# Kernel optimization log

Measured on AMD Instinct MI355X. Metric: run time of the kernel, lower is better.

## Reference

```python
import jax, jax.numpy as jnp
import numpy as np

G = 13            # grid_size
A = 5             # num_anchors
C = 36            # num_classes
OBJ_SCALE = 5.0
NOOBJ_SCALE = 1.0
CLASS_SCALE = 1.0
COORD_SCALE = 1.0
ANCHORS = jnp.array([[1.08, 1.19], [3.42, 4.41], [6.63, 11.38], [9.42, 5.11], [16.62, 10.52]], dtype=jnp.float32)


def setup_inputs() -> dict:
    key = jax.random.key(0)
    k1, k2, k3 = jax.random.split(key, 3)
    B, T = 1024, 30
    predictions = jax.random.normal(k1, (B, A * (5 + C), G, G), dtype=jnp.float32)
    # x,y,w,h normalized to (0,1); class id in [0,C) stored as float in channel 4
    xywh = jax.random.uniform(k2, (B, T, 4), dtype=jnp.float32, minval=1e-3, maxval=0.999)
    cls = jax.random.randint(k3, (B, T, 1), 0, C).astype(jnp.float32)
    target = jnp.concatenate([xywh, cls], axis=-1)
    return {"predictions": predictions, "target": target}


def build_targets(target):
    # target: [B, T, 5]  (x, y, w, h, class), x/y/w/h in [0,1)
    B, T, _ = target.shape
    valid = jnp.sum(target, axis=-1) != 0                      # [B, T]
    gx = target[..., 0] * G
    gy = target[..., 1] * G
    gw = target[..., 2] * G
    gh = target[..., 3] * G
    gi = gx.astype(jnp.int32)                                  # int() truncation (values >= 0)
    gj = gy.astype(jnp.int32)
    # anchor IoU for boxes centered at origin: inter = min(w)*min(h)
    aw = ANCHORS[:, 0]                                          # [A]
    ah = ANCHORS[:, 1]
    inter = jnp.minimum(gw[..., None], aw) * jnp.minimum(gh[..., None], ah)   # [B,T,A]
    union = (gw * gh)[..., None] + aw * ah - inter
    iou = inter / (union + 1e-16)
    best_n = jnp.argmax(iou, axis=-1)                           # [B, T] first-max, matches torch loop
    baw = ANCHORS[best_n, 0]
    bah = ANCHORS[best_n, 1]
    tx = gx - gi.astype(gx.dtype)
    ty = gy - gj.astype(gy.dtype)
    tw = jnp.log(gw / baw + 1e-16)
    th = jnp.log(gh / bah + 1e-16)
    cls_idx = target[..., 4].astype(jnp.int32)                  # [B, T]

    N = B * A * G * G
    b_idx = jnp.arange(B, dtype=jnp.int32)[:, None]             # [B,1] -> broadcast to [B,T]
    flat = ((b_idx * A + best_n.astype(jnp.int32)) * G + gj) * G + gi   # [B,T]
    flat = jnp.where(valid, flat, N)                            # out-of-bounds -> dropped
    flat = flat.reshape(-1)                                     # [B*T]

    conf_mask = jnp.full((N,), NOOBJ_SCALE, dtype=jnp.float32).at[flat].set(OBJ_SCALE, mode="drop")
    coord_mask = jnp.zeros((N, 4), dtype=jnp.float32).at[flat].set(1.0, mode="drop")
    class_mask = jnp.zeros((N, C), dtype=jnp.float32).at[flat].set(CLASS_SCALE, mode="drop")
    tconf = jnp.zeros((N,), dtype=jnp.float32).at[flat].set(1.0, mode="drop")
    tcoord_vals = jnp.stack([tx, ty, tw, th], axis=-1).reshape(-1, 4)
    tcoord = jnp.zeros((N, 4), dtype=jnp.float32).at[flat].set(tcoord_vals, mode="drop")
    tclass = jnp.zeros((N, C), dtype=jnp.float32).at[flat, cls_idx.reshape(-1)].set(1.0, mode="drop")

    shp = (B, A, G, G)
    return (coord_mask.reshape(shp + (4,)), conf_mask.reshape(shp), class_mask.reshape(shp + (C,)),
            tcoord.reshape(shp + (4,)), tconf.reshape(shp), tclass.reshape(shp + (C,)))


def reference(predictions, target):
    B = predictions.shape[0]
    p = predictions.reshape(B, A, 5 + C, G, G).transpose(0, 1, 3, 4, 2)   # [B,A,G,G,5+C]
    coord_mask, conf_mask, class_mask, tcoord, tconf, tclass = build_targets(target)
    pred_coord = p[..., 1:5]
    pred_conf = jax.nn.sigmoid(p[..., 0])
    pred_class = p[..., 5:]
    loss_coord = COORD_SCALE * jnp.sum((pred_coord * coord_mask - tcoord * coord_mask) ** 2) / B
    loss_conf = jnp.sum((pred_conf * conf_mask - tconf * conf_mask) ** 2) / B
    labels = jnp.argmax(tclass.reshape(-1, C), axis=1)
    logp = jax.nn.log_softmax(pred_class.reshape(-1, C), axis=-1)
    loss_class = CLASS_SCALE * (-jnp.take_along_axis(logp, labels[:, None], axis=1).sum()) / B
    total_loss = loss_coord + loss_conf + loss_class
    return (total_loss, loss_coord, loss_conf, loss_class)
```

## Files before the change

### kernel.cpp

```cpp
#include <hip/hip_runtime.h>

#define GQ 13
#define AQ 5
#define CQ 36
#define TQ 30
#define CH (5 + CQ)
#define GG (GQ * GQ)
#define PLANE (CH * GG)
#define BLOCK 256
#define NVEC 6
#define VEC_DWORDS (NVEC * BLOCK * 4)


__global__ __launch_bounds__(BLOCK) void yolo_plane(
    const float* __restrict__ pred,
    const float* __restrict__ target,
    float* __restrict__ ws, int nb)
{
    __shared__ float s_plane[PLANE];
    __shared__ int   s_info[GG];
    __shared__ int   s_cell[TQ];
    __shared__ float s_tc[TQ][4];
    __shared__ int   s_cls[TQ];
    __shared__ float s_red[3][BLOCK / 64];

    const int a   = blockIdx.x;
    const int b   = blockIdx.y;
    const int bid = b * AQ + a;
    const int tid = threadIdx.x;

    const float* src = pred + ((size_t)b * AQ + a) * PLANE;
    float4 vv[NVEC];
    #pragma unroll
    for (int r = 0; r < NVEC; r++)
        __builtin_memcpy(&vv[r], src + (size_t)(tid + BLOCK * r) * 4, 16);
    float tl[4]; int ntl = 0;
    #pragma unroll
    for (int r = 0; r < 4; r++) {
        int i = VEC_DWORDS + tid + BLOCK * r;
        if (i < PLANE) { tl[r] = src[i]; ntl = r + 1; }
    }

    if (tid < TQ) {
        const float* tg = target + ((size_t)b * TQ + tid) * 5;
        float x = tg[0], y = tg[1], w = tg[2], h = tg[3], c5 = tg[4];
        bool valid = (x + y + w + h + c5) != 0.0f;
        float gx = x * GQ, gy = y * GQ, gw = w * GQ, gh = h * GQ;
        int gi = (int)gx, gj = (int)gy;
        const float AW[5] = {1.08f, 3.42f, 6.63f, 9.42f, 16.62f};
        const float AH[5] = {1.19f, 4.41f, 11.38f, 5.11f, 10.52f};
        float best = -1.0f; int bn = 0;
        #pragma unroll
        for (int k = 0; k < AQ; k++) {
            float inter = fminf(gw, AW[k]) * fminf(gh, AH[k]);
            float un    = gw * gh + AW[k] * AH[k] - inter;
            float iou   = inter / (un + 1e-16f);
            if (iou > best) { best = iou; bn = k; }
        }
        s_cell[tid]  = valid ? ((bn * GQ + gj) * GQ + gi) : -1;
        s_tc[tid][0] = gx - (float)gi;
        s_tc[tid][1] = gy - (float)gj;
        s_tc[tid][2] = __logf(gw / AW[bn] + 1e-16f);
        s_tc[tid][3] = __logf(gh / AH[bn] + 1e-16f);
        s_cls[tid]   = (int)c5;
    }
    if (tid < GG) s_info[tid] = 0;

    #pragma unroll
    for (int r = 0; r < NVEC; r++)
        __builtin_memcpy(&s_plane[(tid + BLOCK * r) * 4], &vv[r], 16);
    #pragma unroll
    for (int r = 0; r < 4; r++)
        if (r < ntl) s_plane[VEC_DWORDS + tid + BLOCK * r] = tl[r];
    __syncthreads();

    if (tid == 0) {
        #pragma unroll 1
        for (int t = 0; t < TQ; t++) {
            int c = s_cell[t] - a * GG;
            if (c >= 0 && c < GG) {
                int lab = s_cls[t];
                int old = s_info[c];
                if (old) lab = min(lab, old & 0xff);
                s_info[c] = 0x40000000 | (t << 8) | lab;
            }
        }
    }
    __syncthreads();

    float lcoord = 0.0f, lconf = 0.0f, lclass = 0.0f;
    if (tid < GG) {
        int info = s_info[tid];

        float p0  = s_plane[tid];
        float sig = 1.0f / (1.0f + __expf(-p0));
        float d   = info ? 5.0f * (sig - 1.0f) : sig;
        lconf = d * d;

        if (info) {
            int t = (info >> 8) & 0xff;
            float d1 = s_plane[1 * GG + tid] - s_tc[t][0];
            float d2 = s_plane[2 * GG + tid] - s_tc[t][1];
            float d3 = s_plane[3 * GG + tid] - s_tc[t][2];
            float d4 = s_plane[4 * GG + tid] - s_tc[t][3];
            lcoord = d1 * d1 + d2 * d2 + d3 * d3 + d4 * d4;
        }

        int lab = info & 0xff;
        const float* cb = s_plane + 5 * GG + tid;
        float sum = 0.0f, vl = 0.0f;
        #pragma unroll
        for (int c = 0; c < CQ; c++) {
            float v = cb[(size_t)c * GG];
            sum += __expf(v);
            vl = (c == lab) ? v : vl;
        }
        lclass = __logf(sum) - vl;
    }

    #pragma unroll
    for (int off = 32; off > 0; off >>= 1) {
        lcoord += __shfl_down(lcoord, off, 64);
        lconf  += __shfl_down(lconf,  off, 64);
        lclass += __shfl_down(lclass, off, 64);
    }
    int wv = tid >> 6, ln = tid & 63;
    if (ln == 0) { s_red[0][wv] = lcoord; s_red[1][wv] = lconf; s_red[2][wv] = lclass; }
    __syncthreads();
    if (tid == 0) {
        float a0 = 0.f, a1 = 0.f, a2 = 0.f;
        #pragma unroll
        for (int w = 0; w < BLOCK / 64; w++) {
            a0 += s_red[0][w]; a1 += s_red[1][w]; a2 += s_red[2][w];
        }
        ws[0 * nb + bid] = a0;
        ws[1 * nb + bid] = a1;
        ws[2 * nb + bid] = a2;
    }
}

__global__ __launch_bounds__(BLOCK) void yolo_reduce(
    const float* __restrict__ ws, float* __restrict__ out, int nb, float invB)
{
    __shared__ float s_red[3][BLOCK / 64];
    const int tid = threadIdx.x;
    float a0 = 0.f, a1 = 0.f, a2 = 0.f;
    for (int i = tid; i < nb; i += BLOCK) {
        a0 += ws[0 * nb + i];
        a1 += ws[1 * nb + i];
        a2 += ws[2 * nb + i];
    }
    #pragma unroll
    for (int off = 32; off > 0; off >>= 1) {
        a0 += __shfl_down(a0, off, 64);
        a1 += __shfl_down(a1, off, 64);
        a2 += __shfl_down(a2, off, 64);
    }
    int wv = tid >> 6, ln = tid & 63;
    if (ln == 0) { s_red[0][wv] = a0; s_red[1][wv] = a1; s_red[2][wv] = a2; }
    __syncthreads();
    if (tid == 0) {
        float r0 = 0.f, r1 = 0.f, r2 = 0.f;
        #pragma unroll
        for (int w = 0; w < BLOCK / 64; w++) {
            r0 += s_red[0][w]; r1 += s_red[1][w]; r2 += s_red[2][w];
        }
        r0 *= invB; r1 *= invB; r2 *= invB;
        out[0] = r0 + r1 + r2;
        out[1] = r0;
        out[2] = r1;
        out[3] = r2;
    }
}

extern "C" void kernel_launch(void* const* d_in, const int* in_sizes, int n_in,
                              void* d_out, int out_size, void* d_ws, size_t ws_size,
                              hipStream_t stream)
{
    const float* pred   = (const float*)d_in[0];
    const float* target = (const float*)d_in[1];
    float* out = (float*)d_out;
    float* ws  = (float*)d_ws;

    int B  = in_sizes[0] / (AQ * CH * GG);
    int nb = B * AQ;

    dim3 grid(AQ, B);
    yolo_plane<<<grid, BLOCK, 0, stream>>>(pred, target, ws, nb);
    yolo_reduce<<<1, BLOCK, 0, stream>>>(ws, out, nb, 1.0f / (float)B);
}
```

Measured before the change: 210.9 us.

## Read predictions directly per cell instead of staging planes in shared memory

```diff
diff --git a/kernel.cpp b/kernel.cpp
--- a/kernel.cpp
+++ b/kernel.cpp
@@ -6,40 +6,23 @@
 #define TQ 30
 #define CH (5 + CQ)
 #define GG (GQ * GQ)
-#define PLANE (CH * GG)
+#define CELLS (AQ * GG)
 #define BLOCK 256
-#define NVEC 6
-#define VEC_DWORDS (NVEC * BLOCK * 4)
+#define BPI 4
 
 
-__global__ __launch_bounds__(BLOCK) void yolo_plane(
+__global__ __launch_bounds__(BLOCK) void yolo_cells(
     const float* __restrict__ pred,
     const float* __restrict__ target,
     float* __restrict__ ws, int nb)
 {
-    __shared__ float s_plane[PLANE];
-    __shared__ int   s_info[GG];
-    __shared__ int   s_cell[TQ];
+    __shared__ int   s_pack[TQ];
     __shared__ float s_tc[TQ][4];
-    __shared__ int   s_cls[TQ];
     __shared__ float s_red[3][BLOCK / 64];
 
-    const int a   = blockIdx.x;
     const int b   = blockIdx.y;
-    const int bid = b * AQ + a;
     const int tid = threadIdx.x;
-
-    const float* src = pred + ((size_t)b * AQ + a) * PLANE;
-    float4 vv[NVEC];
-    #pragma unroll
-    for (int r = 0; r < NVEC; r++)
-        __builtin_memcpy(&vv[r], src + (size_t)(tid + BLOCK * r) * 4, 16);
-    float tl[4]; int ntl = 0;
-    #pragma unroll
-    for (int r = 0; r < 4; r++) {
-        int i = VEC_DWORDS + tid + BLOCK * r;
-        if (i < PLANE) { tl[r] = src[i]; ntl = r + 1; }
-    }
+    const int n   = blockIdx.x * BLOCK + tid;
 
     if (tid < TQ) {
         const float* tg = target + ((size_t)b * TQ + tid) * 5;
@@ -57,63 +40,51 @@
             float iou   = inter / (un + 1e-16f);
             if (iou > best) { best = iou; bn = k; }
         }
-        s_cell[tid]  = valid ? ((bn * GQ + gj) * GQ + gi) : -1;
+        int cell = (bn * GQ + gj) * GQ + gi;
+        s_pack[tid]  = valid ? ((cell << 6) | (int)c5) : -1;
         s_tc[tid][0] = gx - (float)gi;
         s_tc[tid][1] = gy - (float)gj;
         s_tc[tid][2] = __logf(gw / AW[bn] + 1e-16f);
         s_tc[tid][3] = __logf(gh / AH[bn] + 1e-16f);
-        s_cls[tid]   = (int)c5;
-    }
-    if (tid < GG) s_info[tid] = 0;
-
-    #pragma unroll
-    for (int r = 0; r < NVEC; r++)
-        __builtin_memcpy(&s_plane[(tid + BLOCK * r) * 4], &vv[r], 16);
-    #pragma unroll
-    for (int r = 0; r < 4; r++)
-        if (r < ntl) s_plane[VEC_DWORDS + tid + BLOCK * r] = tl[r];
-    __syncthreads();
-
-    if (tid == 0) {
-        #pragma unroll 1
-        for (int t = 0; t < TQ; t++) {
-            int c = s_cell[t] - a * GG;
-            if (c >= 0 && c < GG) {
-                int lab = s_cls[t];
-                int old = s_info[c];
-                if (old) lab = min(lab, old & 0xff);
-                s_info[c] = 0x40000000 | (t << 8) | lab;
-            }
-        }
     }
     __syncthreads();
 
     float lcoord = 0.0f, lconf = 0.0f, lclass = 0.0f;
-    if (tid < GG) {
-        int info = s_info[tid];
+    if (n < CELLS) {
+        int a = n / GG;
+        int r = n - a * GG;
+        const float* base = pred + ((size_t)(b * AQ + a) * CH) * GG + r;
 
-        float p0  = s_plane[tid];
+        int mt = -1, minc = 63;
+        #pragma unroll
+        for (int t = 0; t < TQ; t++) {
+            int p = s_pack[t];
+            if ((p >> 6) == n) { mt = t; minc = min(minc, p & 63); }
+        }
+        bool obj = (mt >= 0);
+        int lab  = obj ? minc : 0;
+
+        float p0  = base[0];
         float sig = 1.0f / (1.0f + __expf(-p0));
-        float d   = info ? 5.0f * (sig - 1.0f) : sig;
+        float d   = obj ? 5.0f * (sig - 1.0f) : sig;
         lconf = d * d;
 
-        if (info) {
-            int t = (info >> 8) & 0xff;
-            float d1 = s_plane[1 * GG + tid] - s_tc[t][0];
-            float d2 = s_plane[2 * GG + tid] - s_tc[t][1];
-            float d3 = s_plane[3 * GG + tid] - s_tc[t][2];
-            float d4 = s_plane[4 * GG + tid] - s_tc[t][3];
+        if (obj) {
+            float d1 = base[1 * GG] - s_tc[mt][0];
+            float d2 = base[2 * GG] - s_tc[mt][1];
+            float d3 = base[3 * GG] - s_tc[mt][2];
+            float d4 = base[4 * GG] - s_tc[mt][3];
             lcoord = d1 * d1 + d2 * d2 + d3 * d3 + d4 * d4;
         }
 
-        int lab = info & 0xff;
-        const float* cb = s_plane + 5 * GG + tid;
+        float v[CQ];
+        #pragma unroll
+        for (int c = 0; c < CQ; c++) v[c] = base[(size_t)(5 + c) * GG];
         float sum = 0.0f, vl = 0.0f;
         #pragma unroll
         for (int c = 0; c < CQ; c++) {
-            float v = cb[(size_t)c * GG];
-            sum += __expf(v);
-            vl = (c == lab) ? v : vl;
+            sum += __expf(v[c]);
+            vl = (c == lab) ? v[c] : vl;
         }
         lclass = __logf(sum) - vl;
     }
@@ -133,6 +104,7 @@
         for (int w = 0; w < BLOCK / 64; w++) {
             a0 += s_red[0][w]; a1 += s_red[1][w]; a2 += s_red[2][w];
         }
+        int bid = b * BPI + blockIdx.x;
         ws[0 * nb + bid] = a0;
         ws[1 * nb + bid] = a1;
         ws[2 * nb + bid] = a2;
@@ -183,9 +155,9 @@
     float* ws  = (float*)d_ws;
 
     int B  = in_sizes[0] / (AQ * CH * GG);
-    int nb = B * AQ;
+    int nb = B * BPI;
 
-    dim3 grid(AQ, B);
-    yolo_plane<<<grid, BLOCK, 0, stream>>>(pred, target, ws, nb);
+    dim3 grid(BPI, B);
+    yolo_cells<<<grid, BLOCK, 0, stream>>>(pred, target, ws, nb);
     yolo_reduce<<<1, BLOCK, 0, stream>>>(ws, out, nb, 1.0f / (float)B);
 }
```

New measurement: 207.0 us. About the same (-1.8%).
